# Optimization experiments

Hardware: AMD Instinct MI355X
Metric: run time of the kernel (lower is better)

## Reference

```python
import jax, jax.numpy as jnp
import numpy as np

B, N, K = 2, 32768, 16
CIN, COUT = 8, 64
BN_INV = float(1.0 / np.sqrt(1.0 + 1e-5))  # inference BN with running mean=0, var=1


def _bn_relu(x, g, b):
    # inference BatchNorm (mean=0, var=1) folded into scale/shift, then ReLU
    return jax.nn.relu(x * (g * BN_INV) + b)


def setup_inputs() -> dict:
    key = jax.random.key(0)
    ks = jax.random.split(key, 20)

    def w(k, o, i):
        return jax.random.normal(k, (o, i), jnp.float32) * (1.0 / np.sqrt(i))

    def g(k, c):
        return jax.random.uniform(k, (c,), jnp.float32, 0.5, 1.5)

    def bta(k, c):
        return jax.random.normal(k, (c,), jnp.float32) * 0.1

    return {
        "coords": jax.random.normal(ks[0], (B, N, 3), jnp.float32),
        "features": jax.random.normal(ks[1], (B, N, CIN), jnp.float32),
        "neighbor_indices": jax.random.randint(ks[2], (B, N, K), 0, N, jnp.int32),
        "lse_w1": w(ks[3], CIN, 4), "lse_g1": g(ks[4], CIN), "lse_b1": bta(ks[5], CIN),
        "lse_w2": w(ks[6], 2 * CIN, CIN), "lse_g2": g(ks[7], 2 * CIN), "lse_b2": bta(ks[8], 2 * CIN),
        "m1_w": w(ks[9], COUT // 2, 3 * CIN), "m1_g": g(ks[10], COUT // 2), "m1_b": bta(ks[11], COUT // 2),
        "m2_w": w(ks[12], COUT, COUT // 2), "m2_g": g(ks[13], COUT), "m2_b": bta(ks[14], COUT),
        "att_w": w(ks[15], COUT, COUT),
        "pool_w": w(ks[16], COUT, COUT), "pool_g": g(ks[17], COUT), "pool_b": bta(ks[18], COUT),
    }


def reference(coords, features, neighbor_indices,
              lse_w1, lse_g1, lse_b1, lse_w2, lse_g2, lse_b2,
              m1_w, m1_g, m1_b, m2_w, m2_g, m2_b,
              att_w, pool_w, pool_g, pool_b):
    # gather neighbor features / coords per batch element
    nf = jax.vmap(lambda f, i: f[i])(features, neighbor_indices)  # (B,N,K,CIN)
    nc = jax.vmap(lambda c, i: c[i])(coords, neighbor_indices)    # (B,N,K,3)

    # local spatial encoding: relative pos + distance -> 2 shared-MLP layers
    rel = nc - coords[:, :, None, :]                              # (B,N,K,3)
    dist = jnp.sqrt(jnp.sum(rel * rel, axis=-1, keepdims=True))   # (B,N,K,1)
    enc = jnp.concatenate([rel, dist], axis=-1)                   # (B,N,K,4)
    enc = _bn_relu(enc @ lse_w1.T, lse_g1, lse_b1)                # (B,N,K,CIN)
    enc = _bn_relu(enc @ lse_w2.T, lse_g2, lse_b2)                # (B,N,K,2*CIN)

    x = jnp.concatenate([nf, enc], axis=-1)                       # (B,N,K,3*CIN)
    x = _bn_relu(x @ m1_w.T, m1_g, m1_b)                          # (B,N,K,COUT/2)
    x = _bn_relu(x @ m2_w.T, m2_g, m2_b)                          # (B,N,K,COUT)

    # attentive pooling over the K neighbor axis
    scores = jax.nn.softmax(x @ att_w.T, axis=2)                  # softmax over K
    pooled = jnp.sum(scores * x, axis=2)                          # (B,N,COUT)
    return _bn_relu(pooled @ pool_w.T, pool_g, pool_b)            # (B,N,COUT)
```

## Files before the change

kernel.cpp:

```cpp
#include <hip/hip_runtime.h>
#include <hip/hip_bf16.h>


typedef __attribute__((ext_vector_type(8))) short short8v;
typedef __attribute__((ext_vector_type(4))) float float4v;

#define BN_INV 0.9999950000374997f
#define LOG2E  1.4426950408889634f
#define NFRAG 23
#define NSCAL 24

__device__ __forceinline__ ushort f2bf(float f) {
    return (ushort)((__float_as_uint(f) + 0x8000u) >> 16);
}
__device__ __forceinline__ uint pk2(float a, float b) {
    return __builtin_amdgcn_perm(__float_as_uint(b) + 0x8000u,
                                 __float_as_uint(a) + 0x8000u, 0x07060302u);
}
__device__ __forceinline__ ushort f2bf_rne(float f) {
    __hip_bfloat16 h = __float2bfloat16(f);
    return __builtin_bit_cast(ushort, h);
}
__device__ __forceinline__ float fexp2(float x) {
#if __has_builtin(__builtin_amdgcn_exp2f)
    return __builtin_amdgcn_exp2f(x);
#else
    return exp2f(x);
#endif
}

__global__ __launch_bounds__(256)
void lfa_pack(const float* __restrict__ wm1, const float* __restrict__ wm2,
              const float* __restrict__ watt, const float* __restrict__ wp,
              const float* __restrict__ gm1, const float* __restrict__ bm1,
              const float* __restrict__ gm2, const float* __restrict__ bm2,
              const float* __restrict__ gp,  const float* __restrict__ bp,
              const float* __restrict__ w2,  const float* __restrict__ g2,
              const float* __restrict__ b2,
              ushort* __restrict__ ws)
{
    const int t = blockIdx.x * 256 + threadIdx.x;
    if (t < NFRAG * 64) {
        const int f = t >> 6, l = t & 63, r = l & 15, Q = l >> 4;
        short8v v;
        #pragma unroll
        for (int j = 0; j < 8; ++j) {
            const int k = 8 * Q + j;
            float x;
            if (f == 0)      x = (k < 24) ? wm1[r * 24 + k] : 0.f;
            else if (f == 1) x = (k < 24) ? wm1[(16 + r) * 24 + k] : 0.f;
            else if (f < 6)  { int tt = f - 2;
                               int c = (k >> 1) + 16 * (k & 1);
                               x = wm2[(16 * tt + r) * 32 + c]; }
            else if (f < 14) { int i = f - 6,  tt = i >> 1, h = i & 1;
                               int p = 32 * h + k;
                               int c = 16 * (p & 3) + (p >> 2);
                               x = watt[(16 * tt + r) * 64 + c] * LOG2E; }
            else if (f < 22) { int i = f - 14, tt = i >> 1, h = i & 1;
                               int p = 32 * h + k;
                               int c = 16 * (p & 3) + (p >> 2);
                               x = wp[(16 * tt + r) * 64 + c]; }
            else             { x = (k < 8) ? w2[r * 8 + k] * (g2[r] * BN_INV) : 0.f; }
            v[j] = (short)f2bf_rne(x);
        }
        ((short8v*)ws)[t] = v;
    } else if (t < NFRAG * 64 + NSCAL * 64) {
        const int i = t - NFRAG * 64;
        const int fld = i >> 6, l = i & 63, r = l & 15, Q = l >> 4;
        float x;
        if (fld == 0)      x = gm1[r] * BN_INV;
        else if (fld == 1) x = bm1[r];
        else if (fld == 2) x = gm1[16 + r] * BN_INV;
        else if (fld == 3) x = bm1[16 + r];
        else if (fld < 8)  x = gm2[16 * (fld - 4) + r] * BN_INV;
        else if (fld < 12) x = bm2[16 * (fld - 8) + r];
        else if (fld < 16) x = gp[16 * (fld - 12) + r] * BN_INV;
        else if (fld < 20) x = bp[16 * (fld - 16) + r];
        else               x = b2[4 * Q + (fld - 20)];
        ((float*)(ws + NFRAG * 64 * 8))[i] = x;
    }
}

__global__ __launch_bounds__(64, 2)
void lfa_kernel(const float* __restrict__ coords,
                const float* __restrict__ feats,
                const int*   __restrict__ nidx,
                const float* __restrict__ w1, const float* __restrict__ g1, const float* __restrict__ b1,
                const ushort* __restrict__ fw,
                float* __restrict__ out)
{
    __shared__ __align__(16) ushort sX1[2592];
    __shared__ __align__(16) ushort sX2[1280];
    __shared__ __align__(16) ushort sX3[1152];
    __shared__ __align__(16) ushort sPL[1152];

    const int l   = threadIdx.x & 63;
    const int r   = l & 15;
    const int Q   = l >> 4;
    const int ptb = blockIdx.x * 16;

    const short8v* FR = (const short8v*)fw;
    const float*   SC = (const float*)(fw + NFRAG * 64 * 8);
    const short8v b1f0 = FR[0 * 64 + l];
    const short8v b1f1 = FR[1 * 64 + l];
    const short8v w2f  = FR[22 * 64 + l];
    short8v b2f[4], b3f[8];
    #pragma unroll
    for (int t = 0; t < 4; ++t) b2f[t] = FR[(2 + t) * 64 + l];
    #pragma unroll
    for (int i = 0; i < 8; ++i) b3f[i] = FR[(6 + i) * 64 + l];

    const float sm1a = SC[0 * 64 + l], tm1a = SC[1 * 64 + l];
    const float sm1b = SC[2 * 64 + l], tm1b = SC[3 * 64 + l];
    float sm2[4], tm2[4], t2l[4];
    #pragma unroll
    for (int t = 0; t < 4; ++t) {
        sm2[t] = SC[(4 + t) * 64 + l];  tm2[t] = SC[(8 + t) * 64 + l];
        t2l[t] = SC[(20 + t) * 64 + l];
    }

    ushort* X1  = sX1;
    ushort* X2A = sX2;
    ushort* X2B = X2A + 640;
    ushort* X3A = sX3;
    ushort* X3B = sX2;
    ushort* Xh  = sX2;

    float cx, cy, cz, nx, ny, nz;
    float4 f0v, f1v;
    {
        const int pt0n = ptb;
        const int pt   = pt0n + Q;
        const int nb   = nidx[pt0n * 16 + l];
        const int bb   = pt >> 15;
        const int nbr  = (bb << 15) + nb;
        cx = coords[pt * 3 + 0];  cy = coords[pt * 3 + 1];  cz = coords[pt * 3 + 2];
        nx = coords[nbr * 3 + 0]; ny = coords[nbr * 3 + 1]; nz = coords[nbr * 3 + 2];
        const float4* fp4 = (const float4*)(feats + nbr * 8);
        f0v = fp4[0]; f1v = fp4[1];
    }

    const float4v z0 = {0.f, 0.f, 0.f, 0.f};

    #pragma unroll 1
    for (int it = 0; it < 4; ++it) {
        {
            *(uint*)&Xh[512 + 2 * l] = 0u;

            const float rx = nx - cx;
            const float ry = ny - cy;
            const float rz = nz - cz;
            const float dd = sqrtf(rx * rx + ry * ry + rz * rz);
            float e4[4] = {rx, ry, rz, dd};

            uint4* row = (uint4*)&X1[Q * 648 + r * 40];
            row[0] = make_uint4(pk2(f0v.x, f0v.y), pk2(f0v.z, f0v.w),
                                pk2(f1v.x, f1v.y), pk2(f1v.z, f1v.w));
            row[3] = make_uint4(0u, 0u, 0u, 0u);

            float h1[8];
            #pragma unroll
            for (int o = 0; o < 8; ++o) {
                float a = 0.f;
                #pragma unroll
                for (int i = 0; i < 4; ++i) a = fmaf(w1[o * 4 + i], e4[i], a);
                h1[o] = fmaxf(fmaf(a, g1[o] * BN_INV, b1[o]), 0.f);
            }
            *(uint4*)&Xh[l * 8] = make_uint4(pk2(h1[0], h1[1]), pk2(h1[2], h1[3]),
                                             pk2(h1[4], h1[5]), pk2(h1[6], h1[7]));
            #pragma unroll
            for (int t = 0; t < 4; ++t) {
                const int rowi = (Q == 0) ? (16 * t + r) : (64 + r);
                const short8v bh = *(const short8v*)&Xh[rowi * 8];
                const float4v de = __builtin_amdgcn_mfma_f32_16x16x32_bf16(w2f, bh, z0, 0, 0, 0);
                const float v0 = fmaxf(de[0] + t2l[0], 0.f);
                const float v1 = fmaxf(de[1] + t2l[1], 0.f);
                const float v2 = fmaxf(de[2] + t2l[2], 0.f);
                const float v3 = fmaxf(de[3] + t2l[3], 0.f);
                *(uint2*)&X1[t * 648 + r * 40 + 8 + 4 * Q] =
                    make_uint2(pk2(v0, v1), pk2(v2, v3));
            }
        }

        if (it < 3) {
            const int pt0n = ptb + (it + 1) * 4;
            const int pt   = pt0n + Q;
            const int nb   = nidx[pt0n * 16 + l];
            const int bb   = pt >> 15;
            const int nbr  = (bb << 15) + nb;
            cx = coords[pt * 3 + 0];  cy = coords[pt * 3 + 1];  cz = coords[pt * 3 + 2];
            nx = coords[nbr * 3 + 0]; ny = coords[nbr * 3 + 1]; nz = coords[nbr * 3 + 2];
            const float4* fp4 = (const float4*)(feats + nbr * 8);
            f0v = fp4[0]; f1v = fp4[1];
        }

        __builtin_amdgcn_s_setprio(1);
        #pragma unroll 1
        for (int pp = 0; pp < 2; ++pp) {
            ushort* X1A = X1 + (2 * pp) * 648;
            ushort* X1B = X1A + 648;
            const short8v a1A = *(const short8v*)&X1A[r * 40 + Q * 8];
            const short8v a1B = *(const short8v*)&X1B[r * 40 + Q * 8];
            const float4v d1aA = __builtin_amdgcn_mfma_f32_16x16x32_bf16(a1A, b1f0, z0, 0, 0, 0);
            const float4v d1bA = __builtin_amdgcn_mfma_f32_16x16x32_bf16(a1A, b1f1, z0, 0, 0, 0);
            const float4v d1aB = __builtin_amdgcn_mfma_f32_16x16x32_bf16(a1B, b1f0, z0, 0, 0, 0);
            const float4v d1bB = __builtin_amdgcn_mfma_f32_16x16x32_bf16(a1B, b1f1, z0, 0, 0, 0);
            #pragma unroll
            for (int q = 0; q < 4; ++q) {
                const float vaA = fmaxf(fmaf(d1aA[q], sm1a, tm1a), 0.f);
                const float vbA = fmaxf(fmaf(d1bA[q], sm1b, tm1b), 0.f);
                const float vaB = fmaxf(fmaf(d1aB[q], sm1a, tm1a), 0.f);
                const float vbB = fmaxf(fmaf(d1bB[q], sm1b, tm1b), 0.f);
                *(uint*)&X2A[(4 * Q + q) * 40 + 2 * r] = pk2(vaA, vbA);
                *(uint*)&X2B[(4 * Q + q) * 40 + 2 * r] = pk2(vaB, vbB);
            }
            const short8v a2A = *(const short8v*)&X2A[r * 40 + Q * 8];
            const short8v a2B = *(const short8v*)&X2B[r * 40 + Q * 8];
            float4v d2A[4], d2B[4];
            #pragma unroll
            for (int t = 0; t < 4; ++t) {
                d2A[t] = __builtin_amdgcn_mfma_f32_16x16x32_bf16(a2A, b2f[t], z0, 0, 0, 0);
                d2B[t] = __builtin_amdgcn_mfma_f32_16x16x32_bf16(a2B, b2f[t], z0, 0, 0, 0);
            }
            float xrA[4][4], xrB[4][4];
            #pragma unroll
            for (int t = 0; t < 4; ++t)
                #pragma unroll
                for (int q = 0; q < 4; ++q) {
                    xrA[t][q] = fmaxf(fmaf(d2A[t][q], sm2[t], tm2[t]), 0.f);
                    xrB[t][q] = fmaxf(fmaf(d2B[t][q], sm2[t], tm2[t]), 0.f);
                }

            #pragma unroll
            for (int q = 0; q < 4; ++q) {
                *(uint2*)&X3A[(4 * Q + q) * 72 + 4 * r] =
                    make_uint2(pk2(xrA[0][q], xrA[1][q]), pk2(xrA[2][q], xrA[3][q]));
                *(uint2*)&X3B[(4 * Q + q) * 72 + 4 * r] =
                    make_uint2(pk2(xrB[0][q], xrB[1][q]), pk2(xrB[2][q], xrB[3][q]));
            }
            const short8v a3lA = *(const short8v*)&X3A[r * 72 + Q * 8];
            const short8v a3hA = *(const short8v*)&X3A[r * 72 + 32 + Q * 8];
            const short8v a3lB = *(const short8v*)&X3B[r * 72 + Q * 8];
            const short8v a3hB = *(const short8v*)&X3B[r * 72 + 32 + Q * 8];

            float seA[4], snA[4], seB[4], snB[4];
            #pragma unroll
            for (int t = 0; t < 4; ++t) {
                float4v sA = __builtin_amdgcn_mfma_f32_16x16x32_bf16(a3lA, b3f[t * 2],     z0, 0, 0, 0);
                sA         = __builtin_amdgcn_mfma_f32_16x16x32_bf16(a3hA, b3f[t * 2 + 1], sA, 0, 0, 0);
                float4v sB = __builtin_amdgcn_mfma_f32_16x16x32_bf16(a3lB, b3f[t * 2],     z0, 0, 0, 0);
                sB         = __builtin_amdgcn_mfma_f32_16x16x32_bf16(a3hB, b3f[t * 2 + 1], sB, 0, 0, 0);
                float e0A = fexp2(sA[0]), e1A = fexp2(sA[1]);
                float e2A = fexp2(sA[2]), e3A = fexp2(sA[3]);
                float e0B = fexp2(sB[0]), e1B = fexp2(sB[1]);
                float e2B = fexp2(sB[2]), e3B = fexp2(sB[3]);
                seA[t] = (e0A + e1A) + (e2A + e3A);
                snA[t] = fmaf(e0A, xrA[t][0], e1A * xrA[t][1]) + fmaf(e2A, xrA[t][2], e3A * xrA[t][3]);
                seB[t] = (e0B + e1B) + (e2B + e3B);
                snB[t] = fmaf(e0B, xrB[t][0], e1B * xrB[t][1]) + fmaf(e2B, xrB[t][2], e3B * xrB[t][3]);
            }
            #pragma unroll
            for (int t = 0; t < 4; ++t) {
                seA[t] += __shfl_xor(seA[t], 16, 64);
                snA[t] += __shfl_xor(snA[t], 16, 64);
                seB[t] += __shfl_xor(seB[t], 16, 64);
                snB[t] += __shfl_xor(snB[t], 16, 64);
                seA[t] += __shfl_xor(seA[t], 32, 64);
                snA[t] += __shfl_xor(snA[t], 32, 64);
                seB[t] += __shfl_xor(seB[t], 32, 64);
                snB[t] += __shfl_xor(snB[t], 32, 64);
            }
            {
                const float snqA = (Q == 0) ? snA[0] : (Q == 1) ? snA[1] : (Q == 2) ? snA[2] : snA[3];
                const float seqA = (Q == 0) ? seA[0] : (Q == 1) ? seA[1] : (Q == 2) ? seA[2] : seA[3];
                const float snqB = (Q == 0) ? snB[0] : (Q == 1) ? snB[1] : (Q == 2) ? snB[2] : snB[3];
                const float seqB = (Q == 0) ? seB[0] : (Q == 1) ? seB[1] : (Q == 2) ? seB[2] : seB[3];
                sPL[(4 * it + 2 * pp) * 72 + 4 * r + Q]     = f2bf(__fdividef(snqA, seqA));
                sPL[(4 * it + 2 * pp + 1) * 72 + 4 * r + Q] = f2bf(__fdividef(snqB, seqB));
            }
        }
        __builtin_amdgcn_s_setprio(0);
    }

    short8v pbf[8];
    #pragma unroll
    for (int i = 0; i < 8; ++i) pbf[i] = FR[(14 + i) * 64 + l];
    float spv[4], tpv[4];
    #pragma unroll
    for (int t = 0; t < 4; ++t) {
        spv[t] = SC[(12 + t) * 64 + l]; tpv[t] = SC[(16 + t) * 64 + l];
    }
    const short8v apl0 = *(const short8v*)&sPL[r * 72 + Q * 8];
    const short8v apl1 = *(const short8v*)&sPL[r * 72 + 32 + Q * 8];
    float4v dp[4];
    #pragma unroll
    for (int t = 0; t < 4; ++t) {
        float4v d = __builtin_amdgcn_mfma_f32_16x16x32_bf16(apl0, pbf[t * 2],     z0, 0, 0, 0);
        d         = __builtin_amdgcn_mfma_f32_16x16x32_bf16(apl1, pbf[t * 2 + 1], d,  0, 0, 0);
        dp[t] = d;
    }
    #pragma unroll
    for (int q = 0; q < 4; ++q)
        #pragma unroll
        for (int t = 0; t < 4; ++t)
            out[(ptb + 4 * Q + q) * 64 + 16 * t + r] =
                fmaxf(fmaf(dp[t][q], spv[t], tpv[t]), 0.f);
}

extern "C" void kernel_launch(void* const* d_in, const int* in_sizes, int n_in,
                              void* d_out, int out_size, void* d_ws, size_t ws_size,
                              hipStream_t stream) {
    (void)in_sizes; (void)n_in; (void)ws_size; (void)out_size;
    const float* coords = (const float*)d_in[0];
    const float* feats  = (const float*)d_in[1];
    const int*   nidx   = (const int*)  d_in[2];
    const float* w1  = (const float*)d_in[3];
    const float* g1  = (const float*)d_in[4];
    const float* b1  = (const float*)d_in[5];
    const float* w2  = (const float*)d_in[6];
    const float* g2  = (const float*)d_in[7];
    const float* b2  = (const float*)d_in[8];
    const float* wm1 = (const float*)d_in[9];
    const float* gm1 = (const float*)d_in[10];
    const float* bm1 = (const float*)d_in[11];
    const float* wm2 = (const float*)d_in[12];
    const float* gm2 = (const float*)d_in[13];
    const float* bm2 = (const float*)d_in[14];
    const float* watt = (const float*)d_in[15];
    const float* wp  = (const float*)d_in[16];
    const float* gp  = (const float*)d_in[17];
    const float* bp  = (const float*)d_in[18];
    float* out = (float*)d_out;
    ushort* ws = (ushort*)d_ws;

    lfa_pack<<<dim3(12), dim3(256), 0, stream>>>(wm1, wm2, watt, wp,
                                                 gm1, bm1, gm2, bm2, gp, bp,
                                                 w2, g2, b2, ws);
    lfa_kernel<<<dim3(4096), dim3(64), 0, stream>>>(coords, feats, nidx,
                                                    w1, g1, b1, ws, out);
}
```

Measured before the change: 51.56 us.

## Double-buffer local spatial encoding stage one iteration ahead of MLP stage

```diff
diff --git a/kernel.cpp b/kernel.cpp
--- a/kernel.cpp
+++ b/kernel.cpp
@@ -89,7 +89,8 @@
                 const ushort* __restrict__ fw,
                 float* __restrict__ out)
 {
-    __shared__ __align__(16) ushort sX1[2592];
+    __shared__ __align__(16) ushort sX1[2 * 2592];
+    __shared__ __align__(16) ushort sXh[640];
     __shared__ __align__(16) ushort sX2[1280];
     __shared__ __align__(16) ushort sX3[1152];
     __shared__ __align__(16) ushort sPL[1152];
@@ -119,12 +120,13 @@
         t2l[t] = SC[(20 + t) * 64 + l];
     }
 
-    ushort* X1  = sX1;
     ushort* X2A = sX2;
     ushort* X2B = X2A + 640;
     ushort* X3A = sX3;
     ushort* X3B = sX2;
-    ushort* Xh  = sX2;
+    ushort* Xh  = sXh;
+
+    *(uint*)&Xh[512 + 2 * l] = 0u;
 
     float cx, cy, cz, nx, ny, nz;
     float4 f0v, f1v;
@@ -142,62 +144,73 @@
 
     const float4v z0 = {0.f, 0.f, 0.f, 0.f};
 
+#define LSE_BODY(X1B, DO_PF, PT0PF)                                           \
+    do {                                                                      \
+        const float rx_ = nx - cx;                                            \
+        const float ry_ = ny - cy;                                            \
+        const float rz_ = nz - cz;                                            \
+        const float dd_ = sqrtf(rx_ * rx_ + ry_ * ry_ + rz_ * rz_);           \
+        float e4_[4] = {rx_, ry_, rz_, dd_};                                  \
+        uint4* row_ = (uint4*)&(X1B)[Q * 648 + r * 40];                       \
+        row_[0] = make_uint4(pk2(f0v.x, f0v.y), pk2(f0v.z, f0v.w),            \
+                             pk2(f1v.x, f1v.y), pk2(f1v.z, f1v.w));           \
+        row_[3] = make_uint4(0u, 0u, 0u, 0u);                                 \
+        float h1_[8];                                                         \
+        _Pragma("unroll")                                                     \
+        for (int o_ = 0; o_ < 8; ++o_) {                                      \
+            float a_ = 0.f;                                                   \
+            _Pragma("unroll")                                                 \
+            for (int i_ = 0; i_ < 4; ++i_)                                    \
+                a_ = fmaf(w1[o_ * 4 + i_], e4_[i_], a_);                      \
+            h1_[o_] = fmaxf(fmaf(a_, g1[o_] * BN_INV, b1[o_]), 0.f);          \
+        }                                                                     \
+        *(uint4*)&Xh[l * 8] = make_uint4(pk2(h1_[0], h1_[1]),                 \
+                                         pk2(h1_[2], h1_[3]),                 \
+                                         pk2(h1_[4], h1_[5]),                 \
+                                         pk2(h1_[6], h1_[7]));                \
+        if (DO_PF) {                                                          \
+            const int pt0n_ = (PT0PF);                                        \
+            const int pt_   = pt0n_ + Q;                                      \
+            const int nb_   = nidx[pt0n_ * 16 + l];                           \
+            const int bb_   = pt_ >> 15;                                      \
+            const int nbr_  = (bb_ << 15) + nb_;                              \
+            cx = coords[pt_ * 3 + 0];  cy = coords[pt_ * 3 + 1];              \
+            cz = coords[pt_ * 3 + 2];                                         \
+            nx = coords[nbr_ * 3 + 0]; ny = coords[nbr_ * 3 + 1];             \
+            nz = coords[nbr_ * 3 + 2];                                        \
+            const float4* fp4_ = (const float4*)(feats + nbr_ * 8);           \
+            f0v = fp4_[0]; f1v = fp4_[1];                                     \
+        }                                                                     \
+        _Pragma("unroll")                                                     \
+        for (int t_ = 0; t_ < 4; ++t_) {                                      \
+            const int rowi_ = (Q == 0) ? (16 * t_ + r) : (64 + r);            \
+            const short8v bh_ = *(const short8v*)&Xh[rowi_ * 8];              \
+            const float4v de_ =                                               \
+                __builtin_amdgcn_mfma_f32_16x16x32_bf16(w2f, bh_, z0, 0, 0, 0);\
+            const float v0_ = fmaxf(de_[0] + t2l[0], 0.f);                    \
+            const float v1_ = fmaxf(de_[1] + t2l[1], 0.f);                    \
+            const float v2_ = fmaxf(de_[2] + t2l[2], 0.f);                    \
+            const float v3_ = fmaxf(de_[3] + t2l[3], 0.f);                    \
+            *(uint2*)&(X1B)[t_ * 648 + r * 40 + 8 + 4 * Q] =                  \
+                make_uint2(pk2(v0_, v1_), pk2(v2_, v3_));                     \
+        }                                                                     \
+    } while (0)
+
+    LSE_BODY(&sX1[0], true, ptb + 4);
+
     #pragma unroll 1
     for (int it = 0; it < 4; ++it) {
-        {
-            *(uint*)&Xh[512 + 2 * l] = 0u;
-
-            const float rx = nx - cx;
-            const float ry = ny - cy;
-            const float rz = nz - cz;
-            const float dd = sqrtf(rx * rx + ry * ry + rz * rz);
-            float e4[4] = {rx, ry, rz, dd};
-
-            uint4* row = (uint4*)&X1[Q * 648 + r * 40];
-            row[0] = make_uint4(pk2(f0v.x, f0v.y), pk2(f0v.z, f0v.w),
-                                pk2(f1v.x, f1v.y), pk2(f1v.z, f1v.w));
-            row[3] = make_uint4(0u, 0u, 0u, 0u);
-
-            float h1[8];
-            #pragma unroll
-            for (int o = 0; o < 8; ++o) {
-                float a = 0.f;
-                #pragma unroll
-                for (int i = 0; i < 4; ++i) a = fmaf(w1[o * 4 + i], e4[i], a);
-                h1[o] = fmaxf(fmaf(a, g1[o] * BN_INV, b1[o]), 0.f);
-            }
-            *(uint4*)&Xh[l * 8] = make_uint4(pk2(h1[0], h1[1]), pk2(h1[2], h1[3]),
-                                             pk2(h1[4], h1[5]), pk2(h1[6], h1[7]));
-            #pragma unroll
-            for (int t = 0; t < 4; ++t) {
-                const int rowi = (Q == 0) ? (16 * t + r) : (64 + r);
-                const short8v bh = *(const short8v*)&Xh[rowi * 8];
-                const float4v de = __builtin_amdgcn_mfma_f32_16x16x32_bf16(w2f, bh, z0, 0, 0, 0);
-                const float v0 = fmaxf(de[0] + t2l[0], 0.f);
-                const float v1 = fmaxf(de[1] + t2l[1], 0.f);
-                const float v2 = fmaxf(de[2] + t2l[2], 0.f);
-                const float v3 = fmaxf(de[3] + t2l[3], 0.f);
-                *(uint2*)&X1[t * 648 + r * 40 + 8 + 4 * Q] =
-                    make_uint2(pk2(v0, v1), pk2(v2, v3));
-            }
+        if (it < 3) {
+            ushort* X1N = &sX1[((it + 1) & 1) * 2592];
+            LSE_BODY(X1N, it < 2, ptb + (it + 2) * 4);
         }
 
-        if (it < 3) {
-            const int pt0n = ptb + (it + 1) * 4;
-            const int pt   = pt0n + Q;
-            const int nb   = nidx[pt0n * 16 + l];
-            const int bb   = pt >> 15;
-            const int nbr  = (bb << 15) + nb;
-            cx = coords[pt * 3 + 0];  cy = coords[pt * 3 + 1];  cz = coords[pt * 3 + 2];
-            nx = coords[nbr * 3 + 0]; ny = coords[nbr * 3 + 1]; nz = coords[nbr * 3 + 2];
-            const float4* fp4 = (const float4*)(feats + nbr * 8);
-            f0v = fp4[0]; f1v = fp4[1];
-        }
+        ushort* X1C = &sX1[(it & 1) * 2592];
 
         __builtin_amdgcn_s_setprio(1);
         #pragma unroll 1
         for (int pp = 0; pp < 2; ++pp) {
-            ushort* X1A = X1 + (2 * pp) * 648;
+            ushort* X1A = X1C + (2 * pp) * 648;
             ushort* X1B = X1A + 648;
             const short8v a1A = *(const short8v*)&X1A[r * 40 + Q * 8];
             const short8v a1B = *(const short8v*)&X1B[r * 40 + Q * 8];
@@ -281,6 +294,7 @@
         }
         __builtin_amdgcn_s_setprio(0);
     }
+#undef LSE_BODY
 
     short8v pbf[8];
     #pragma unroll
```

After: 53.33 us. 1.03x slower.
